# Kernel optimization log

Measured on AMD Instinct MI355X. Metric: run time of the kernel, lower is better.

## Reference

```python
import jax, jax.numpy as jnp
import numpy as np

B, N, C_IN, C_OUT = 16, 1024, 256, 256
POOL_RATIO = 0.5  # pooling_ration


def setup_inputs() -> dict:
    key = jax.random.key(0)
    k0, k1, k2, k3 = jax.random.split(key, 4)
    x = jax.random.normal(k0, (B, N, C_IN), dtype=jnp.float32)
    # sparse-ish dense adjacency (as the module stores adj densely)
    adj = (jax.random.uniform(k1, (B, N, N)) < 0.02).astype(jnp.float32)
    mask = jnp.ones((B, N), dtype=jnp.int32)
    n_nodes = jnp.full((B,), N, dtype=jnp.int32)
    stdv = 1.0 / np.sqrt(C_IN)
    W = jax.random.uniform(k2, (C_IN, C_OUT), minval=-stdv, maxval=stdv, dtype=jnp.float32)
    b = jnp.zeros((C_OUT,), dtype=jnp.float32)
    pooling = jax.random.uniform(k3, (C_OUT, 1), minval=-1.0, maxval=1.0, dtype=jnp.float32)
    return {"x": x, "adj": adj, "mask": mask, "n_nodes": n_nodes, "W": W, "b": b, "pooling": pooling}


def reference(x, adj, mask, n_nodes, W, b, pooling):
    # GraphConvolutionLayer: adj @ (x W) + b   (standard Kipf GCN layer)
    h = jnp.einsum('bnm,bmc->bnc', adj, x @ W) + b          # [B,N,C_OUT]
    Bm, Nm, C = h.shape
    # projection score y = (h @ pooling) / ||pooling||
    y = (h.reshape(Bm * Nm, C) @ pooling).reshape(Bm, Nm)
    y = y / jnp.sqrt(jnp.sum(pooling ** 2))
    # ascending sort indices
    idx = jnp.argsort(y, axis=1)                            # [B,N]
    n_remove = (n_nodes.astype(jnp.float32) * (1.0 - POOL_RATIO)).astype(jnp.int32)
    new_n_nodes = n_nodes - n_remove
    # vectorized equivalent of the per-batch loop: among currently-masked nodes
    # (in ascending-score order), zero out the first n_remove[b] of them.
    m_sorted = jnp.take_along_axis(mask, idx, axis=1)       # mask gathered in sorted order
    rank = jnp.cumsum(m_sorted, axis=1) - m_sorted          # exclusive rank among masked
    remove = (m_sorted == 1) & (rank < n_remove[:, None])
    new_sorted = jnp.where(remove, 0, m_sorted)
    inv = jnp.argsort(idx, axis=1)                          # inverse permutation
    new_mask = jnp.take_along_axis(new_sorted, inv, axis=1)  # [B,N] int
    mf = new_mask.astype(h.dtype)
    x_out = h * jnp.tanh(y)[:, :, None] * mf[:, :, None]
    adj_out = mf[:, :, None] * adj * mf[:, None, :]
    return x_out, adj_out, new_mask, new_n_nodes
```

## Files before the change

kernel.cpp:

```cpp
#include <hip/hip_runtime.h>
#include <math.h>

#define Bsz 16
#define Nn  1024

#define ADJ_OFF    (16*1024*256)
#define MASK_OFF   (ADJ_OFF + 16*1024*1024)
#define NN_OFF     (MASK_OFF + 16*1024)

typedef unsigned long long u64;
typedef unsigned short u16;
typedef short bf16x8 __attribute__((ext_vector_type(8)));
typedef float f32x4  __attribute__((ext_vector_type(4)));

static __device__ inline u16 f2bf(float f) {
    unsigned u = __float_as_uint(f);
    u += 0x7fffu + ((u >> 16) & 1u);
    return (u16)(u >> 16);
}

static __device__ inline u64 spread4(u64 x) {
    x &= 0xFFFFULL;
    x = (x | (x << 24)) & 0x000000FF000000FFULL;
    x = (x | (x << 12)) & 0x000F000F000F000FULL;
    x = (x | (x << 6))  & 0x0303030303030303ULL;
    x = (x | (x << 3))  & 0x1111111111111111ULL;
    return x;
}

static __device__ inline bf16x8 expand8(unsigned kb) {
    union { unsigned u[4]; bf16x8 v; } r;
    #pragma unroll
    for (int p = 0; p < 4; ++p) {
        unsigned lo = (kb >> (2 * p)) & 1u;
        unsigned hi = (kb >> (2 * p + 1)) & 1u;
        r.u[p] = (lo ? 0x3F80u : 0u) | (hi ? 0x3F800000u : 0u);
    }
    return r.v;
}

__global__ __launch_bounds__(256) void k1(const float* __restrict__ x,
                                          const float* __restrict__ W,
                                          const float* __restrict__ pool,
                                          u16* __restrict__ XB,
                                          u16* __restrict__ WT,
                                          float* __restrict__ Z) {
    int bid = blockIdx.x, t = threadIdx.x, lane = t & 63, wid = t >> 6;
    if (bid < 256) {
        __shared__ float sp[256];
        __shared__ float swp[256];
        sp[t] = pool[t];
        __syncthreads();
        float acc = 0.f;
        const float* wr = W + t * 256;
        for (int j = 0; j < 256; j += 4) {
            float4 w4 = *(const float4*)&wr[j];
            acc = fmaf(w4.x, sp[j], fmaf(w4.y, sp[j + 1],
                  fmaf(w4.z, sp[j + 2], fmaf(w4.w, sp[j + 3], acc))));
        }
        swp[t] = acc;
        __syncthreads();
        const float* w4p = &swp[lane * 4];
        float wx = w4p[0], wy = w4p[1], wz = w4p[2], ww = w4p[3];
        int base = bid * 64 + wid * 16;
        #pragma unroll 1
        for (int rb = 0; rb < 4; ++rb) {
            float4 v[4];
            #pragma unroll
            for (int k = 0; k < 4; ++k)
                v[k] = ((const float4*)(x + (size_t)(base + rb * 4 + k) * 256))[lane];
            #pragma unroll
            for (int k = 0; k < 4; ++k) {
                int row = base + rb * 4 + k;
                ushort4 o;
                o.x = f2bf(v[k].x); o.y = f2bf(v[k].y); o.z = f2bf(v[k].z); o.w = f2bf(v[k].w);
                ((ushort4*)(XB + (size_t)row * 256))[lane] = o;
                float a = fmaf(v[k].x, wx, fmaf(v[k].y, wy, fmaf(v[k].z, wz, v[k].w * ww)));
                for (int off = 32; off > 0; off >>= 1) a += __shfl_down(a, off, 64);
                if (lane == 0) Z[row] = a;
            }
        }
    } else {
        __shared__ float sT[64][65];
        int bt = bid - 256;
        int tr = (bt >> 2) * 64, tc = (bt & 3) * 64;
        #pragma unroll
        for (int p = 0; p < 4; ++p) {
            int r = p * 16 + (t >> 4), c = (t & 15) * 4;
            float4 w = *(const float4*)&W[(size_t)(tr + r) * 256 + tc + c];
            sT[r][c] = w.x; sT[r][c + 1] = w.y; sT[r][c + 2] = w.z; sT[r][c + 3] = w.w;
        }
        __syncthreads();
        #pragma unroll
        for (int p = 0; p < 2; ++p) {
            int nl = p * 32 + (t >> 3), kl = (t & 7) * 8;
            u16 tmp[8];
            #pragma unroll
            for (int j = 0; j < 8; ++j) tmp[j] = f2bf(sT[kl + j][nl]);
            *(int4*)&WT[(size_t)(tc + nl) * 256 + tr + kl] = *(const int4*)tmp;
        }
    }
}

__global__ __launch_bounds__(256) void k2(const u16* __restrict__ XB,
                                          const u16* __restrict__ WT,
                                          const float* __restrict__ adj,
                                          const float* __restrict__ Z,
                                          u16* __restrict__ XWBT,
                                          u64* __restrict__ ABITS,
                                          float* __restrict__ Y) {
    int t = threadIdx.x, lane = t & 63, wid = t >> 6;
    if (blockIdx.x < 256) {
        __shared__ __align__(16) short sT[128][136];
        int idx = blockIdx.x;
        int b  = (idx & 7) + ((idx >> 7) << 3);
        int tl = (idx >> 3) & 15;
        int bm = (b << 3) + (tl >> 1);
        int bn = tl & 1;
        int wr = (wid >> 1) * 64, wc = (wid & 1) * 64;
        int fm = lane & 15, fq = lane >> 4;

        f32x4 acc[4][4];
        #pragma unroll
        for (int i = 0; i < 4; ++i)
            #pragma unroll
            for (int j = 0; j < 4; ++j)
                acc[i][j] = (f32x4){0.f, 0.f, 0.f, 0.f};

        const u16* baseA = XB + ((size_t)(bm * 128)) * 256;
        const u16* baseB = WT + ((size_t)(bn * 128)) * 256;

        #pragma unroll 1
        for (int kt = 0; kt < 4; ++kt) {
            #pragma unroll
            for (int ks = 0; ks < 64; ks += 32) {
                int ko = kt * 64 + ks + fq * 8;
                bf16x8 af[4], bfv[4];
                #pragma unroll
                for (int i = 0; i < 4; ++i)
                    af[i] = *(const bf16x8*)&baseA[(size_t)(wr + i * 16 + fm) * 256 + ko];
                #pragma unroll
                for (int j = 0; j < 4; ++j)
                    bfv[j] = *(const bf16x8*)&baseB[(size_t)(wc + j * 16 + fm) * 256 + ko];
                __builtin_amdgcn_s_setprio(1);
                #pragma unroll
                for (int i = 0; i < 4; ++i)
                    #pragma unroll
                    for (int j = 0; j < 4; ++j)
                        acc[i][j] = __builtin_amdgcn_mfma_f32_16x16x32_bf16(af[i], bfv[j], acc[i][j], 0, 0, 0);
                __builtin_amdgcn_s_setprio(0);
            }
        }
        #pragma unroll
        for (int i = 0; i < 4; ++i) {
            int m = wr + i * 16 + fq * 4;
            #pragma unroll
            for (int j = 0; j < 4; ++j) {
                int c = wc + j * 16 + fm;
                #pragma unroll
                for (int r = 0; r < 4; ++r)
                    sT[c][m + r] = (short)f2bf(acc[i][j][r]);
            }
        }
        __syncthreads();
        u16* dst = XWBT + (size_t)b * 262144 + (size_t)(bn * 128) * 1024 + (bm & 7) * 128;
        int cl = t >> 4, mo = (t & 15) * 8;
        #pragma unroll
        for (int p = 0; p < 8; ++p) {
            int c = p * 16 + cl;
            *(int4*)&dst[(size_t)c * 1024 + mo] = *(const int4*)&sT[c][mo];
        }
    } else {
        int g = blockIdx.x - 256;
        int b = (g & 7) + ((g >> 9) << 3);
        int grp = (g >> 3) & 63;
        __shared__ float sZ[1024];
        ((float4*)sZ)[t] = ((const float4*)(Z + (b << 10)))[t];
        __syncthreads();
        const float* z0 = &sZ[lane * 4];
        #pragma unroll 1
        for (int rr = 0; rr < 4; ++rr) {
            int row = (b << 10) + grp * 16 + wid * 4 + rr;
            const float4* ar = (const float4*)(adj + (size_t)row * 1024);
            float4 v0 = ar[lane], v1 = ar[64 + lane], v2 = ar[128 + lane], v3 = ar[192 + lane];
            u64 B00 = __ballot(v0.x != 0.f), B01 = __ballot(v0.y != 0.f);
            u64 B02 = __ballot(v0.z != 0.f), B03 = __ballot(v0.w != 0.f);
            u64 B10 = __ballot(v1.x != 0.f), B11 = __ballot(v1.y != 0.f);
            u64 B12 = __ballot(v1.z != 0.f), B13 = __ballot(v1.w != 0.f);
            u64 B20 = __ballot(v2.x != 0.f), B21 = __ballot(v2.y != 0.f);
            u64 B22 = __ballot(v2.z != 0.f), B23 = __ballot(v2.w != 0.f);
            u64 B30 = __ballot(v3.x != 0.f), B31 = __ballot(v3.y != 0.f);
            u64 B32 = __ballot(v3.z != 0.f), B33 = __ballot(v3.w != 0.f);
            u64 t0, t1, t2, t3;
            int c = (lane >> 2) & 3;
            if (c == 0)      { t0 = B00; t1 = B01; t2 = B02; t3 = B03; }
            else if (c == 1) { t0 = B10; t1 = B11; t2 = B12; t3 = B13; }
            else if (c == 2) { t0 = B20; t1 = B21; t2 = B22; t3 = B23; }
            else             { t0 = B30; t1 = B31; t2 = B32; t3 = B33; }
            int sh = (lane & 3) * 16;
            u64 wbits = spread4(t0 >> sh) | (spread4(t1 >> sh) << 1)
                      | (spread4(t2 >> sh) << 2) | (spread4(t3 >> sh) << 3);
            if (lane < 16) ABITS[(size_t)row * 16 + lane] = wbits;
            float a = v0.x * z0[0] + v0.y * z0[1] + v0.z * z0[2] + v0.w * z0[3];
            a += v1.x * z0[256] + v1.y * z0[257] + v1.z * z0[258] + v1.w * z0[259];
            a += v2.x * z0[512] + v2.y * z0[513] + v2.z * z0[514] + v2.w * z0[515];
            a += v3.x * z0[768] + v3.y * z0[769] + v3.z * z0[770] + v3.w * z0[771];
            for (int off = 32; off > 0; off >>= 1) a += __shfl_down(a, off, 64);
            if (lane == 0) Y[row] = a;
        }
    }
}

__device__ inline u64 shfl_xor_u64(u64 v, int m) {
    int lo = __shfl_xor((int)(v & 0xffffffffULL), m, 64);
    int hi = __shfl_xor((int)(v >> 32), m, 64);
    return ((u64)(unsigned)hi << 32) | (unsigned)lo;
}

__global__ __launch_bounds__(1024) void k3(const float* __restrict__ Y,
                                           const int* __restrict__ maskIn,
                                           const int* __restrict__ nNodes,
                                           const float* __restrict__ bias,
                                           const float* __restrict__ pool,
                                           float* __restrict__ SCALE,
                                           float* __restrict__ NM,
                                           float* __restrict__ newN,
                                           u64* __restrict__ NMBITS) {
    __shared__ u64 s[1024];
    __shared__ int wsum[16];
    __shared__ int nmLoc[1024];
    __shared__ float redb[4], redq[4];
    __shared__ float sBP, sINV;

    int b = blockIdx.x, t = threadIdx.x, lane = t & 63, wid = t >> 6;
    int base = b << 10;

    if (t < 256) {
        float pv = pool[t];
        float bv = bias[t] * pv;
        float qv = pv * pv;
        for (int off = 32; off > 0; off >>= 1) {
            bv += __shfl_down(bv, off, 64);
            qv += __shfl_down(qv, off, 64);
        }
        if (lane == 0) { redb[wid] = bv; redq[wid] = qv; }
    }
    __syncthreads();
    if (t == 0) {
        sBP  = redb[0] + redb[1] + redb[2] + redb[3];
        sINV = 1.0f / sqrtf(redq[0] + redq[1] + redq[2] + redq[3]);
    }

    float ky = Y[base + t];
    unsigned u = __float_as_uint(ky);
    u = (u & 0x80000000u) ? ~u : (u | 0x80000000u);
    u64 val = ((u64)u << 32) | (unsigned)t;

    for (int k = 2; k <= 1024; k <<= 1) {
        bool up = ((t & k) == 0);
        int j = k >> 1;
        for (; j >= 64; j >>= 1) {
            s[t] = val; __syncthreads();
            u64 p = s[t ^ j]; __syncthreads();
            bool keepMin = (up == ((t & j) == 0));
            bool pLess = p < val;
            val = (keepMin == pLess) ? p : val;
        }
        for (; j >= 1; j >>= 1) {
            u64 p = shfl_xor_u64(val, j);
            bool keepMin = (up == ((t & j) == 0));
            bool pLess = p < val;
            val = (keepMin == pLess) ? p : val;
        }
    }

    int idx = (int)(val & 1023u);
    int mval = maskIn[base + idx];
    int sc = mval;
    for (int off = 1; off < 64; off <<= 1) {
        int nv = __shfl_up(sc, off, 64);
        if (lane >= off) sc += nv;
    }
    if (lane == 63) wsum[wid] = sc;
    __syncthreads();
    int offset = 0;
    for (int w = 0; w < wid; ++w) offset += wsum[w];
    int rank = sc + offset - mval;
    int nn = nNodes[b];
    int nrem = (int)((float)nn * 0.5f);
    int nm = (mval == 1 && rank < nrem) ? 0 : mval;
    nmLoc[idx] = nm;
    NM[base + idx] = (float)nm;
    if (t == 0) newN[b] = (float)(nn - nrem);
    __syncthreads();

    int myNm = nmLoc[t];
    u64 bmask = __ballot(myNm != 0);
    if (lane == 0) NMBITS[b * 16 + wid] = bmask;
    float yr = Y[base + t];
    SCALE[base + t] = myNm ? tanhf((yr + sBP) * sINV) : 0.0f;
}

__global__ __launch_bounds__(256) void k4(const u64* __restrict__ ABITS,
                                          const u16* __restrict__ XWBT,
                                          const float* __restrict__ SCALE,
                                          const float* __restrict__ bias,
                                          const u64* __restrict__ NMBITS,
                                          float* __restrict__ XO,
                                          float* __restrict__ AO) {
    int t = threadIdx.x, lane = t & 63, wid = t >> 6;
    if (blockIdx.x < 256) {
        __shared__ u64 sBitsA[128][18];
        int idx = blockIdx.x;
        int b   = (idx & 7) + ((idx >> 7) << 3);
        int tl  = (idx >> 3) & 15;
        int bmt = tl >> 1, bn = tl & 1;
        int wr = (wid >> 1) * 64, wc = (wid & 1) * 64;
        int fm = lane & 15, fq = lane >> 4;

        {
            int r = t >> 1, hq = (t & 1) * 8;
            const u64* src = ABITS + ((size_t)(b * 1024 + bmt * 128 + r)) * 16 + hq;
            #pragma unroll
            for (int q = 0; q < 8; q += 2) {
                ulonglong2 v = *(const ulonglong2*)&src[q];
                sBitsA[r][hq + q] = v.x;
                sBitsA[r][hq + q + 1] = v.y;
            }
        }

        f32x4 acc[4][4];
        #pragma unroll
        for (int i = 0; i < 4; ++i)
            #pragma unroll
            for (int j = 0; j < 4; ++j)
                acc[i][j] = (f32x4){0.f, 0.f, 0.f, 0.f};

        const u16* baseB = XWBT + (size_t)b * 262144 + (size_t)(bn * 128) * 1024;
        __syncthreads();

        #pragma unroll 1
        for (int kt = 0; kt < 16; ++kt) {
            u64 rb[4];
            #pragma unroll
            for (int i = 0; i < 4; ++i)
                rb[i] = sBitsA[wr + i * 16 + fm][kt];
            #pragma unroll
            for (int ks = 0; ks < 64; ks += 32) {
                bf16x8 af[4], bfv[4];
                #pragma unroll
                for (int j = 0; j < 4; ++j)
                    bfv[j] = *(const bf16x8*)&baseB[(size_t)(wc + j * 16 + fm) * 1024 + kt * 64 + ks + fq * 8];
                #pragma unroll
                for (int i = 0; i < 4; ++i)
                    af[i] = expand8((unsigned)(rb[i] >> (ks + fq * 8)) & 0xFFu);
                __builtin_amdgcn_s_setprio(1);
                #pragma unroll
                for (int i = 0; i < 4; ++i)
                    #pragma unroll
                    for (int j = 0; j < 4; ++j)
                        acc[i][j] = __builtin_amdgcn_mfma_f32_16x16x32_bf16(af[i], bfv[j], acc[i][j], 0, 0, 0);
                __builtin_amdgcn_s_setprio(0);
            }
        }
        float bj[4];
        #pragma unroll
        for (int j = 0; j < 4; ++j) bj[j] = bias[bn * 128 + wc + j * 16 + fm];
        int mb = (b << 10) + bmt * 128 + wr;
        #pragma unroll
        for (int i = 0; i < 4; ++i) {
            int m0 = mb + i * 16 + fq * 4;
            float s0 = SCALE[m0], s1 = SCALE[m0 + 1], s2 = SCALE[m0 + 2], s3 = SCALE[m0 + 3];
            #pragma unroll
            for (int j = 0; j < 4; ++j) {
                int c = bn * 128 + wc + j * 16 + fm;
                float* xo = XO + (size_t)m0 * 256 + c;
                xo[0]   = (acc[i][j][0] + bj[j]) * s0;
                xo[256] = (acc[i][j][1] + bj[j]) * s1;
                xo[512] = (acc[i][j][2] + bj[j]) * s2;
                xo[768] = (acc[i][j][3] + bj[j]) * s3;
            }
        }
    } else {
        int g = blockIdx.x - 256;
        int b = (g & 7) + ((g >> 9) << 3);
        int grp = (g >> 3) & 63;
        __shared__ u64 sNMB[16];
        __shared__ u64 sRB[16][17];
        if (t < 16) sNMB[t] = NMBITS[b * 16 + t];
        sRB[t >> 4][t & 15] = ABITS[((size_t)((b << 10) + grp * 16 + (t >> 4))) * 16 + (t & 15)];
        __syncthreads();
        int c0 = t * 4;
        u64 wb = sNMB[c0 >> 6] >> (c0 & 63);
        float m0 = (wb & 1) ? 1.f : 0.f;
        float m1 = ((wb >> 1) & 1) ? 1.f : 0.f;
        float m2 = ((wb >> 2) & 1) ? 1.f : 0.f;
        float m3 = ((wb >> 3) & 1) ? 1.f : 0.f;
        #pragma unroll 1
        for (int r = 0; r < 16; ++r) {
            int rloc = grp * 16 + r;
            int nmRow = (int)((sNMB[rloc >> 6] >> (rloc & 63)) & 1ULL);
            float4* aor = (float4*)(AO + (size_t)((b << 10) + rloc) * 1024);
            if (nmRow) {
                unsigned rbits = (unsigned)(sRB[r][t >> 4] >> (4 * (t & 15))) & 0xFu;
                float4 o;
                o.x = (rbits & 1u) ? m0 : 0.f;
                o.y = (rbits & 2u) ? m1 : 0.f;
                o.z = (rbits & 4u) ? m2 : 0.f;
                o.w = (rbits & 8u) ? m3 : 0.f;
                aor[t] = o;
            } else {
                aor[t] = make_float4(0.f, 0.f, 0.f, 0.f);
            }
        }
    }
}

extern "C" void kernel_launch(void* const* d_in, const int* in_sizes, int n_in,
                              void* d_out, int out_size, void* d_ws, size_t ws_size,
                              hipStream_t stream) {
    const float* x      = (const float*)d_in[0];
    const float* adj    = (const float*)d_in[1];
    const int*   mask   = (const int*)d_in[2];
    const int*   nnodes = (const int*)d_in[3];
    const float* W      = (const float*)d_in[4];
    const float* bias   = (const float*)d_in[5];
    const float* pool   = (const float*)d_in[6];

    float* out = (float*)d_out;
    float* XO  = out;
    float* AO  = out + ADJ_OFF;
    float* NM  = out + MASK_OFF;
    float* NNo = out + NN_OFF;

    char* w = (char*)d_ws;
    u16*   XB     = (u16*)(w);
    u16*   WT     = (u16*)(w + 8388608);
    u16*   XWBT   = (u16*)(w + 8519680);
    u64*   ABITS  = (u64*)(w + 16908288);
    float* Z      = (float*)(w + 19005440);
    float* Y      = (float*)(w + 19070976);
    float* SCALE  = (float*)(w + 19136512);
    u64*   NMBITS = (u64*)(w + 19202048);

    k1<<<272, 256, 0, stream>>>(x, W, pool, XB, WT, Z);
    k2<<<1280, 256, 0, stream>>>(XB, WT, adj, Z, XWBT, ABITS, Y);
    k3<<<Bsz, 1024, 0, stream>>>(Y, mask, nnodes, bias, pool, SCALE, NM, NNo, NMBITS);
    k4<<<1280, 256, 0, stream>>>(ABITS, XWBT, SCALE, bias, NMBITS, XO, AO);
}
```

Baseline: 203.4 us.

## Replace bitonic sort with radix-select threshold for top-k mask

The full 1024-element bitonic sort per batch, which needed many shared-memory rounds with barriers, is replaced by a 6-pass 7-bit radix select. The select finds the key of the n_remove-th smallest masked node, and each node then compares its own 42-bit key (score bits plus index) against that threshold. This removes the sort and the inverse-permutation scatter, in exchange for shared-memory atomics and histogram scans. k3 is a small kernel, so the effect on total time is limited.

Result: no change. 200.5 us, median of 2 (-1.4%).

```diff
diff --git a/kernel.cpp b/kernel.cpp
--- a/kernel.cpp
+++ b/kernel.cpp
@@ -211,12 +211,6 @@
     }
 }
 
-__device__ inline u64 shfl_xor_u64(u64 v, int m) {
-    int lo = __shfl_xor((int)(v & 0xffffffffULL), m, 64);
-    int hi = __shfl_xor((int)(v >> 32), m, 64);
-    return ((u64)(unsigned)hi << 32) | (unsigned)lo;
-}
-
 __global__ __launch_bounds__(1024) void k3(const float* __restrict__ Y,
                                            const int* __restrict__ maskIn,
                                            const int* __restrict__ nNodes,
@@ -226,11 +220,11 @@
                                            float* __restrict__ NM,
                                            float* __restrict__ newN,
                                            u64* __restrict__ NMBITS) {
-    __shared__ u64 s[1024];
-    __shared__ int wsum[16];
-    __shared__ int nmLoc[1024];
+    __shared__ int sHist[128];
+    __shared__ int sScan[2];
+    __shared__ int wsumM[16];
     __shared__ float redb[4], redq[4];
-    __shared__ float sBP, sINV;
+    __shared__ int sSel, sTgt;
 
     int b = blockIdx.x, t = threadIdx.x, lane = t & 63, wid = t >> 6;
     int base = b << 10;
@@ -245,60 +239,66 @@
         }
         if (lane == 0) { redb[wid] = bv; redq[wid] = qv; }
     }
-    __syncthreads();
-    if (t == 0) {
-        sBP  = redb[0] + redb[1] + redb[2] + redb[3];
-        sINV = 1.0f / sqrtf(redq[0] + redq[1] + redq[2] + redq[3]);
-    }
 
     float ky = Y[base + t];
     unsigned u = __float_as_uint(ky);
     u = (u & 0x80000000u) ? ~u : (u | 0x80000000u);
-    u64 val = ((u64)u << 32) | (unsigned)t;
-
-    for (int k = 2; k <= 1024; k <<= 1) {
-        bool up = ((t & k) == 0);
-        int j = k >> 1;
-        for (; j >= 64; j >>= 1) {
-            s[t] = val; __syncthreads();
-            u64 p = s[t ^ j]; __syncthreads();
-            bool keepMin = (up == ((t & j) == 0));
-            bool pLess = p < val;
-            val = (keepMin == pLess) ? p : val;
-        }
-        for (; j >= 1; j >>= 1) {
-            u64 p = shfl_xor_u64(val, j);
-            bool keepMin = (up == ((t & j) == 0));
-            bool pLess = p < val;
-            val = (keepMin == pLess) ? p : val;
-        }
-    }
-
-    int idx = (int)(val & 1023u);
-    int mval = maskIn[base + idx];
-    int sc = mval;
-    for (int off = 1; off < 64; off <<= 1) {
-        int nv = __shfl_up(sc, off, 64);
-        if (lane >= off) sc += nv;
-    }
-    if (lane == 63) wsum[wid] = sc;
+    int mval = maskIn[base + t];
+    u64 ck = ((u64)u << 10) | (unsigned)t;
+
+    int ms = mval;
+    for (int off = 32; off > 0; off >>= 1) ms += __shfl_down(ms, off, 64);
+    if (lane == 0) wsumM[wid] = ms;
     __syncthreads();
-    int offset = 0;
-    for (int w = 0; w < wid; ++w) offset += wsum[w];
-    int rank = sc + offset - mval;
+
+    float sBP  = redb[0] + redb[1] + redb[2] + redb[3];
+    float sINV = 1.0f / sqrtf(redq[0] + redq[1] + redq[2] + redq[3]);
+    int mtotal = 0;
+    #pragma unroll
+    for (int w = 0; w < 16; ++w) mtotal += wsumM[w];
+
     int nn = nNodes[b];
     int nrem = (int)((float)nn * 0.5f);
-    int nm = (mval == 1 && rank < nrem) ? 0 : mval;
-    nmLoc[idx] = nm;
-    NM[base + idx] = (float)nm;
+
+    u64 T;
+    if (nrem >= mtotal) {
+        T = ~0ULL;
+    } else {
+        u64 prefix = 0;
+        int target = nrem;
+        for (int r = 0; r < 6; ++r) {
+            int shift = 35 - 7 * r;
+            if (t < 128) sHist[t] = 0;
+            __syncthreads();
+            bool active = (mval != 0) && ((ck >> (shift + 7)) == prefix);
+            if (active) atomicAdd(&sHist[(int)((ck >> shift) & 127)], 1);
+            __syncthreads();
+            int x = 0, v = 0;
+            if (t < 128) {
+                v = sHist[t];
+                x = v;
+                for (int o = 1; o < 64; o <<= 1) { int n = __shfl_up(x, o, 64); if (lane >= o) x += n; }
+                if (lane == 63) sScan[t >> 6] = x;
+            }
+            __syncthreads();
+            if (t < 128) {
+                int incl = x + ((t >= 64) ? sScan[0] : 0);
+                int excl = incl - v;
+                if (excl <= target && target < incl) { sSel = t; sTgt = target - excl; }
+            }
+            __syncthreads();
+            prefix = (prefix << 7) | (unsigned)sSel;
+            target = sTgt;
+        }
+        T = prefix;
+    }
+
+    int nm = (mval == 1 && ck < T) ? 0 : mval;
+    NM[base + t] = (float)nm;
+    u64 bmask = __ballot(nm != 0);
+    if (lane == 0) NMBITS[b * 16 + wid] = bmask;
+    SCALE[base + t] = nm ? tanhf((ky + sBP) * sINV) : 0.0f;
     if (t == 0) newN[b] = (float)(nn - nrem);
-    __syncthreads();
-
-    int myNm = nmLoc[t];
-    u64 bmask = __ballot(myNm != 0);
-    if (lane == 0) NMBITS[b * 16 + wid] = bmask;
-    float yr = Y[base + t];
-    SCALE[base + t] = myNm ? tanhf((yr + sBP) * sINV) : 0.0f;
 }
 
 __global__ __launch_bounds__(256) void k4(const u64* __restrict__ ABITS,
```
